# Optimization experiments

Hardware: AMD Instinct MI355X
Metric: run time of the kernel (lower is better)

The kernel has to match this reference:

```python
import jax, jax.numpy as jnp
import numpy as np

NHEAD = 8
LN_EPS = 1e-5


def _layernorm(x, g, b):
    mu = jnp.mean(x, -1, keepdims=True)
    var = jnp.mean((x - mu) ** 2, -1, keepdims=True)
    return (x - mu) / jnp.sqrt(var + LN_EPS) * g + b


def _sparse_attn(q, k, v, P):
    # Topology: P queries attend to P keys; G queries attend to P keys + self.
    # q,k,v: [B,H,L,dh], keys/values restricted to pcpt block [B,H,P,dh]
    dh = q.shape[-1]
    scale = 1.0 / jnp.sqrt(jnp.asarray(dh, q.dtype))
    kp, vp = k[:, :, :P], v[:, :, :P]
    S = jnp.einsum('bhld,bhpd->bhlp', q, kp) * scale  # [B,H,L,P]
    # pcpt queries: plain softmax over P keys
    out_p = jnp.einsum('bhqp,bhpd->bhqd', jax.nn.softmax(S[:, :, :P], axis=-1), vp)
    # gen queries: P keys + own diagonal key
    qg, kg, vg = q[:, :, P:], k[:, :, P:], v[:, :, P:]
    Sg = S[:, :, P:]                                   # [B,H,G,P]
    dlog = jnp.sum(qg * kg, -1) * scale                # [B,H,G] diagonal logits
    m = jnp.maximum(jnp.max(Sg, -1), dlog)
    eg = jnp.exp(Sg - m[..., None])
    ed = jnp.exp(dlog - m)
    den = jnp.sum(eg, -1) + ed
    out_g = (jnp.einsum('bhgp,bhpd->bhgd', eg, vp) + ed[..., None] * vg) / den[..., None]
    return jnp.concatenate([out_p, out_g], axis=2)     # [B,H,L,dh]


def _forward(pcpt, gen, Wqkv, bqkv, Wo, bo, W1, b1, W2, b2, g1, beta1, g2, beta2):
    P = pcpt.shape[1]
    x = jnp.concatenate([pcpt, gen], axis=1)           # [B,L,d]
    B, L, d = x.shape
    dh = d // NHEAD
    for i in range(Wqkv.shape[0]):  # post-norm layers
        qkv = (x @ Wqkv[i] + bqkv[i]).reshape(B, L, 3, NHEAD, dh)
        q = jnp.transpose(qkv[:, :, 0], (0, 2, 1, 3))
        k = jnp.transpose(qkv[:, :, 1], (0, 2, 1, 3))
        v = jnp.transpose(qkv[:, :, 2], (0, 2, 1, 3))
        a = _sparse_attn(q, k, v, P)
        a = jnp.transpose(a, (0, 2, 1, 3)).reshape(B, L, d)
        a = a @ Wo[i] + bo[i]
        x = _layernorm(x + a, g1[i], beta1[i])
        h = jax.nn.relu(x @ W1[i] + b1[i]) @ W2[i] + b2[i]
        x = _layernorm(x + h, g2[i], beta2[i])
    return x


def setup_inputs() -> dict:
    key = jax.random.key(0)
    ks = jax.random.split(key, 16)
    B, P, G, d, ff, Lyr = 4, 1024, 1024, 512, 2048, 4
    s = 0.02
    f32 = jnp.float32
    return {
        'pcpt_total_embs': jax.random.normal(ks[0], (B, P, d), f32),
        'gen_total_embs': jax.random.normal(ks[1], (B, G, d), f32),
        'src_key_padding_mask': jnp.zeros((B, P + G), bool),
        'Wqkv': jax.random.normal(ks[2], (Lyr, d, 3 * d), f32) * s,
        'bqkv': jnp.zeros((Lyr, 3 * d), f32),
        'Wo': jax.random.normal(ks[3], (Lyr, d, d), f32) * s,
        'bo': jnp.zeros((Lyr, d), f32),
        'W1': jax.random.normal(ks[4], (Lyr, d, ff), f32) * s,
        'b1': jnp.zeros((Lyr, ff), f32),
        'W2': jax.random.normal(ks[5], (Lyr, ff, d), f32) * s,
        'b2': jnp.zeros((Lyr, d), f32),
        'g1': jnp.ones((Lyr, d), f32),
        'beta1': jnp.zeros((Lyr, d), f32),
        'g2': jnp.ones((Lyr, d), f32),
        'beta2': jnp.zeros((Lyr, d), f32),
    }


def reference(pcpt_total_embs, gen_total_embs, src_key_padding_mask, Wqkv, bqkv, Wo, bo, W1, b1, W2, b2, g1, beta1, g2, beta2):
    P = pcpt_total_embs.shape[1]
    x = _forward(pcpt_total_embs, gen_total_embs, Wqkv, bqkv, Wo, bo, W1, b1, W2, b2, g1, beta1, g2, beta2)
    return x[:, :P], x[:, P:]
```

## Files before the change

### kernel.cpp

```cpp
#include <hip/hip_runtime.h>
#include <hip/hip_bf16.h>

#define B_ 4
#define P_ 1024
#define G_ 1024
#define L_ 2048
#define D_ 512
#define FF_ 2048
#define H_ 8
#define DH_ 64
#define LAYERS_ 4
#define LN_EPS_ 1e-5f

typedef __attribute__((ext_vector_type(8))) short bf16x8;
typedef __attribute__((ext_vector_type(4))) float f32x4;

__device__ __forceinline__ ushort f2b(float f) {
  unsigned u = __float_as_uint(f);
  unsigned r = (u + 0x7fffu + ((u >> 16) & 1u)) >> 16;
  return (ushort)r;
}
__device__ __forceinline__ float b2f(ushort u) {
  return __uint_as_float(((unsigned)u) << 16);
}

__device__ __forceinline__ void gld16(const ushort* g, ushort* l) {
  __builtin_amdgcn_global_load_lds(
      (const __attribute__((address_space(1))) void*)g,
      (__attribute__((address_space(3))) void*)l, 16, 0, 0);
}

__global__ __launch_bounds__(256) void concat_kernel(const float* __restrict__ p,
    const float* __restrict__ g, float* __restrict__ x, ushort* __restrict__ xb)
{
  const int LD4 = L_*D_/4, PD4 = P_*D_/4;
  int i = blockIdx.x*256 + threadIdx.x;
  int b = i / LD4, r = i - b*LD4;
  float4 v;
  if (r < PD4) v = ((const float4*)p)[(size_t)b*PD4 + r];
  else         v = ((const float4*)g)[(size_t)b*PD4 + (r-PD4)];
  ((float4*)x)[i] = v;
  ushort4 h; h.x=f2b(v.x); h.y=f2b(v.y); h.z=f2b(v.z); h.w=f2b(v.w);
  ((ushort4*)xb)[i] = h;
}

__global__ __launch_bounds__(256) void writeout_kernel(const float* __restrict__ x,
    float* __restrict__ out)
{
  const int LD4 = L_*D_/4, PD4 = P_*D_/4, HALF = B_*PD4;
  int i = blockIdx.x*256 + threadIdx.x;
  int half = (i >= HALF) ? 1 : 0;
  int r = i - half*HALF;
  int b = r / PD4, q = r - b*PD4;
  ((float4*)out)[i] = ((const float4*)x)[(size_t)b*LD4 + half*PD4 + q];
}

__global__ __launch_bounds__(256) void wconv_kernel(const float* __restrict__ src,
    ushort* __restrict__ dst, int K, int N)
{
  __shared__ float tile[32][33];
  int n0 = blockIdx.x*32, k0 = blockIdx.y*32, l = blockIdx.z;
  src += (size_t)l*K*N; dst += (size_t)l*K*N;
  int tx = threadIdx.x & 31, ty = threadIdx.x >> 5;
  #pragma unroll
  for (int u=0;u<4;++u) tile[ty+8*u][tx] = src[(size_t)(k0+ty+8*u)*N + n0+tx];
  __syncthreads();
  #pragma unroll
  for (int u=0;u<4;++u) dst[(size_t)(n0+ty+8*u)*K + k0+tx] = f2b(tile[tx][ty+8*u]);
}

template<int BN_, int RELU, int RES, int OUTBF>
__global__ __launch_bounds__(256) void mgemm(
    const ushort* __restrict__ A, const ushort* __restrict__ Bt,
    const float* __restrict__ bias, const float* __restrict__ res,
    void* __restrict__ Cout, int M, int N, int K)
{
  constexpr int MI = (BN_ == 128) ? 4 : 2;
  constexpr int BL = BN_ / 32;
  __shared__ ushort As[128*64];
  __shared__ ushort Bs[BN_*64];
  int t = threadIdx.x;
  int lane = t & 63, w = t >> 6;
  int wm = (BN_ == 128) ? (w >> 1) * 64 : w * 32;
  int wn = (BN_ == 128) ? (w & 1) * 64 : 0;
  int m0 = blockIdx.x * 128, n0 = blockIdx.y * BN_;

  f32x4 acc[MI][4] = {};

  int rbase = t >> 3;
  int cch   = (t & 7) ^ ((t >> 3) & 7);
  const ushort* Ag = A  + (size_t)(m0 + rbase)*K + cch*8;
  const ushort* Bg = Bt + (size_t)(n0 + rbase)*K + cch*8;
  ushort* Asl = As + t*8;
  ushort* Bsl = Bs + t*8;
  const size_t rowK32 = (size_t)32 * K;

  int fr = lane & 15, fq = lane >> 4;
  int swr[2];
  swr[0] = ((0*4 + fq) ^ (fr & 7)) * 8;
  swr[1] = ((1*4 + fq) ^ (fr & 7)) * 8;
  const ushort* Ard = As + (wm + fr)*64;
  const ushort* Brd = Bs + (wn + fr)*64;

  for (int k0 = 0; k0 < K; k0 += 64) {
    __syncthreads();
    #pragma unroll
    for (int L = 0; L < 4; ++L)  gld16(Ag + L*rowK32, Asl + L*2048);
    #pragma unroll
    for (int L = 0; L < BL; ++L) gld16(Bg + L*rowK32, Bsl + L*2048);
    Ag += 64; Bg += 64;
    __syncthreads();
    #pragma unroll
    for (int s = 0; s < 2; ++s) {
      int sw = swr[s];
      bf16x8 af[MI], bfr[4];
      #pragma unroll
      for (int i=0;i<MI;++i) af[i]  = *(const bf16x8*)(Ard + i*16*64 + sw);
      #pragma unroll
      for (int j=0;j<4;++j)  bfr[j] = *(const bf16x8*)(Brd + j*16*64 + sw);
      #pragma unroll
      for (int i=0;i<MI;++i)
        #pragma unroll
        for (int j=0;j<4;++j)
          acc[i][j] = __builtin_amdgcn_mfma_f32_16x16x32_bf16(af[i], bfr[j], acc[i][j], 0, 0, 0);
    }
  }

  int ncol = lane & 15;
  int rquad = (lane >> 4) * 4;
  #pragma unroll
  for (int j=0;j<4;++j) {
    int n = n0 + wn + j*16 + ncol;
    float bv = bias[n];
    #pragma unroll
    for (int i=0;i<MI;++i) {
      int mbase = m0 + wm + i*16 + rquad;
      #pragma unroll
      for (int r=0;r<4;++r) {
        int m = mbase + r;
        float c = acc[i][j][r] + bv;
        if (RES) c += res[(size_t)m*N + n];
        if (RELU) c = fmaxf(c, 0.f);
        if (OUTBF) ((ushort*)Cout)[(size_t)m*N + n] = f2b(c);
        else       ((float*)Cout)[(size_t)m*N + n] = c;
      }
    }
  }
}

__global__ __launch_bounds__(256) void mgemm_qkv(
    const ushort* __restrict__ A,
    const ushort* __restrict__ Bt,
    const float* __restrict__ bias,
    ushort* __restrict__ qb,
    ushort* __restrict__ kb,
    ushort* __restrict__ vtb)
{
  const int K = D_;
  __shared__ ushort As[128*64];
  __shared__ ushort Bs[128*64];
  int t = threadIdx.x;
  int lane = t & 63, w = t >> 6;
  int wm = (w >> 1) * 64, wn = (w & 1) * 64;
  int m0 = blockIdx.x * 128, n0 = blockIdx.y * 128;

  f32x4 acc[4][4] = {};

  int rbase = t >> 3;
  int cch   = (t & 7) ^ ((t >> 3) & 7);
  const ushort* Ag = A  + (size_t)(m0 + rbase)*K + cch*8;
  const ushort* Bg = Bt + (size_t)(n0 + rbase)*K + cch*8;
  ushort* Asl = As + t*8;
  ushort* Bsl = Bs + t*8;
  const size_t rowK32 = (size_t)32 * K;

  int fr = lane & 15, fq = lane >> 4;
  int swr[2];
  swr[0] = ((0*4 + fq) ^ (fr & 7)) * 8;
  swr[1] = ((1*4 + fq) ^ (fr & 7)) * 8;
  const ushort* Ard = As + (wm + fr)*64;
  const ushort* Brd = Bs + (wn + fr)*64;

  for (int k0 = 0; k0 < K; k0 += 64) {
    __syncthreads();
    #pragma unroll
    for (int L = 0; L < 4; ++L) gld16(Ag + L*rowK32, Asl + L*2048);
    #pragma unroll
    for (int L = 0; L < 4; ++L) gld16(Bg + L*rowK32, Bsl + L*2048);
    Ag += 64; Bg += 64;
    __syncthreads();
    #pragma unroll
    for (int s = 0; s < 2; ++s) {
      int sw = swr[s];
      bf16x8 af[4], bfr[4];
      #pragma unroll
      for (int i=0;i<4;++i) af[i]  = *(const bf16x8*)(Ard + i*16*64 + sw);
      #pragma unroll
      for (int j=0;j<4;++j) bfr[j] = *(const bf16x8*)(Brd + j*16*64 + sw);
      #pragma unroll
      for (int i=0;i<4;++i)
        #pragma unroll
        for (int j=0;j<4;++j)
          acc[i][j] = __builtin_amdgcn_mfma_f32_16x16x32_bf16(af[i], bfr[j], acc[i][j], 0, 0, 0);
    }
  }

  int ncol = lane & 15;
  int rquad = (lane >> 4) * 4;
  #pragma unroll
  for (int j=0;j<4;++j) {
    int n = n0 + wn + j*16 + ncol;
    float bv = bias[n];
    int part = n >> 9;
    int wi = n & 511;
    int h = wi >> 6, d = wi & 63;
    #pragma unroll
    for (int i=0;i<4;++i) {
      int mbase = m0 + wm + i*16 + rquad;
      #pragma unroll
      for (int r=0;r<4;++r) {
        int m = mbase + r;
        int b = m >> 11, l = m & 2047;
        int bh = b*H_ + h;
        float cv = acc[i][j][r] + bv;
        if (part == 0) cv *= 0.125f;
        ushort c = f2b(cv);
        if (part == 0)      qb[((size_t)bh*L_ + l)*DH_ + d] = c;
        else if (part == 1) kb[((size_t)bh*L_ + l)*DH_ + d] = c;
        else                vtb[((size_t)bh*DH_ + d)*L_ + l] = c;
      }
    }
  }
}

__global__ __launch_bounds__(256) void attn_mfma(
    const ushort* __restrict__ qb, const ushort* __restrict__ kb,
    const ushort* __restrict__ vtb, ushort* __restrict__ outa)
{
  __shared__ ushort Qs[64*72];
  __shared__ ushort Ks[64*72];
  __shared__ ushort Vts[64*72];
  __shared__ ushort Ps[4*16*72];
  __shared__ float dls[64];

  int t = threadIdx.x;
  int lane = t & 63, w = t >> 6;
  int qt = blockIdx.x & 31;
  int h  = (blockIdx.x >> 5) & 7;
  int b  = blockIdx.x >> 8;
  int l0 = qt * 64;
  bool isgen = (l0 >= P_);
  int bh = b*H_ + h;

  const ushort* qg  = qb  + ((size_t)bh*L_ + l0)*DH_;
  const ushort* kgb = kb  + (size_t)bh*L_*DH_;
  const ushort* vtg = vtb + (size_t)bh*DH_*L_;

  int sr = t >> 3, sc = (t & 7) * 8;

  {
    uint4 x0 = *(const uint4*)(qg + (size_t)sr*DH_ + sc);
    uint4 x1 = *(const uint4*)(qg + (size_t)(sr+32)*DH_ + sc);
    *(uint4*)(Qs + sr*72 + sc) = x0;
    *(uint4*)(Qs + (sr+32)*72 + sc) = x1;
  }
  __syncthreads();

  int fr = lane & 15, fq = lane >> 4;
  bf16x8 qf[2];
  qf[0] = *(const bf16x8*)(Qs + (16*w + fr)*72 + 0*32 + fq*8);
  qf[1] = *(const bf16x8*)(Qs + (16*w + fr)*72 + 1*32 + fq*8);

  float den[4] = {0.f, 0.f, 0.f, 0.f};
  f32x4 o[4] = {};

  ushort* Pw = Ps + w*16*72;

  uint4 pk0 = *(const uint4*)(kgb + (size_t)sr*DH_ + sc);
  uint4 pk1 = *(const uint4*)(kgb + (size_t)(sr+32)*DH_ + sc);
  uint4 pv0 = *(const uint4*)(vtg + (size_t)sr*L_ + sc);
  uint4 pv1 = *(const uint4*)(vtg + (size_t)(sr+32)*L_ + sc);

  for (int kt = 0; kt < 16; ++kt) {
    __syncthreads();
    *(uint4*)(Ks + sr*72 + sc) = pk0;
    *(uint4*)(Ks + (sr+32)*72 + sc) = pk1;
    *(uint4*)(Vts + sr*72 + sc) = pv0;
    *(uint4*)(Vts + (sr+32)*72 + sc) = pv1;
    __syncthreads();

    if (kt < 15) {
      int p1 = (kt + 1) * 64;
      pk0 = *(const uint4*)(kgb + (size_t)(p1+sr)*DH_ + sc);
      pk1 = *(const uint4*)(kgb + (size_t)(p1+sr+32)*DH_ + sc);
      pv0 = *(const uint4*)(vtg + (size_t)sr*L_ + p1 + sc);
      pv1 = *(const uint4*)(vtg + (size_t)(sr+32)*L_ + p1 + sc);
    }

    f32x4 sc4[4] = {};
    #pragma unroll
    for (int s=0;s<2;++s) {
      #pragma unroll
      for (int j=0;j<4;++j) {
        bf16x8 kf = *(const bf16x8*)(Ks + (j*16 + fr)*72 + s*32 + fq*8);
        sc4[j] = __builtin_amdgcn_mfma_f32_16x16x32_bf16(qf[s], kf, sc4[j], 0, 0, 0);
      }
    }

    #pragma unroll
    for (int r=0;r<4;++r) {
      float e0 = __expf(sc4[0][r]);
      float e1 = __expf(sc4[1][r]);
      float e2 = __expf(sc4[2][r]);
      float e3 = __expf(sc4[3][r]);
      den[r] += (e0+e1) + (e2+e3);
      Pw[(fq*4+r)*72 +  0 + fr] = (ushort)(__float_as_uint(e0) >> 16);
      Pw[(fq*4+r)*72 + 16 + fr] = (ushort)(__float_as_uint(e1) >> 16);
      Pw[(fq*4+r)*72 + 32 + fr] = (ushort)(__float_as_uint(e2) >> 16);
      Pw[(fq*4+r)*72 + 48 + fr] = (ushort)(__float_as_uint(e3) >> 16);
    }
    asm volatile("s_waitcnt lgkmcnt(0)" ::: "memory");

    #pragma unroll
    for (int s=0;s<2;++s) {
      bf16x8 pf = *(const bf16x8*)(Pw + fr*72 + s*32 + fq*8);
      #pragma unroll
      for (int j=0;j<4;++j) {
        bf16x8 vf = *(const bf16x8*)(Vts + (j*16 + fr)*72 + s*32 + fq*8);
        o[j] = __builtin_amdgcn_mfma_f32_16x16x32_bf16(pf, vf, o[j], 0, 0, 0);
      }
    }
  }

  #pragma unroll
  for (int r=0;r<4;++r) {
    float d = den[r];
    d += __shfl_xor(d, 1, 16);
    d += __shfl_xor(d, 2, 16);
    d += __shfl_xor(d, 4, 16);
    d += __shfl_xor(d, 8, 16);
    den[r] = d;
  }

  if (isgen) {
    __syncthreads();
    {
      uint4 k0v = *(const uint4*)(kgb + (size_t)(l0+sr)*DH_ + sc);
      uint4 k1v = *(const uint4*)(kgb + (size_t)(l0+sr+32)*DH_ + sc);
      uint4 v0v = *(const uint4*)(vtg + (size_t)sr*L_ + l0 + sc);
      uint4 v1v = *(const uint4*)(vtg + (size_t)(sr+32)*L_ + l0 + sc);
      *(uint4*)(Ks + sr*72 + sc) = k0v;
      *(uint4*)(Ks + (sr+32)*72 + sc) = k1v;
      *(uint4*)(Vts + sr*72 + sc) = v0v;
      *(uint4*)(Vts + (sr+32)*72 + sc) = v1v;
    }
    __syncthreads();
    {
      int row = t >> 2, part = t & 3;
      float dsum = 0.f;
      #pragma unroll
      for (int u=0;u<16;++u) {
        int d = part*16 + u;
        dsum = fmaf(b2f(Qs[row*72+d]), b2f(Ks[row*72+d]), dsum);
      }
      dsum += __shfl_xor(dsum, 1, 4);
      dsum += __shfl_xor(dsum, 2, 4);
      if (part == 0) dls[row] = dsum;
    }
    __syncthreads();
    #pragma unroll
    for (int r=0;r<4;++r) {
      int rr = 16*w + fq*4 + r;
      float ed = __expf(dls[rr]);
      den[r] += ed;
      #pragma unroll
      for (int j=0;j<4;++j) {
        float vv = b2f(Vts[(j*16 + fr)*72 + rr]);
        o[j][r] += ed*vv;
      }
    }
  }

  #pragma unroll
  for (int r=0;r<4;++r) {
    float inv = 1.f / den[r];
    int l = l0 + 16*w + fq*4 + r;
    #pragma unroll
    for (int j=0;j<4;++j)
      outa[((size_t)b*L_ + l)*D_ + h*DH_ + j*16 + fr] = f2b(o[j][r]*inv);
  }
}

__global__ __launch_bounds__(64) void ln_kernel(const float* __restrict__ y,
    const float* __restrict__ gw, const float* __restrict__ bw,
    float* __restrict__ x, ushort* __restrict__ xb)
{
  int row = blockIdx.x, t = threadIdx.x;
  const float4* yr = (const float4*)(y + (size_t)row*D_);
  float4 v0 = yr[t], v1 = yr[t+64];
  float s = v0.x+v0.y+v0.z+v0.w + v1.x+v1.y+v1.z+v1.w;
  for (int off=32; off>0; off>>=1) s += __shfl_down(s, off, 64);
  s = __shfl(s, 0, 64);
  float mu = s * (1.f/D_);
  float dx;
  float q = 0.f;
  dx=v0.x-mu; q+=dx*dx; dx=v0.y-mu; q+=dx*dx; dx=v0.z-mu; q+=dx*dx; dx=v0.w-mu; q+=dx*dx;
  dx=v1.x-mu; q+=dx*dx; dx=v1.y-mu; q+=dx*dx; dx=v1.z-mu; q+=dx*dx; dx=v1.w-mu; q+=dx*dx;
  for (int off=32; off>0; off>>=1) q += __shfl_down(q, off, 64);
  q = __shfl(q, 0, 64);
  float rinv = rsqrtf(q*(1.f/D_) + LN_EPS_);
  const float4* g4 = (const float4*)gw;
  const float4* b4 = (const float4*)bw;
  float4 gv0=g4[t], gv1=g4[t+64], bv0=b4[t], bv1=b4[t+64];
  float4 o0, o1;
  o0.x=(v0.x-mu)*rinv*gv0.x+bv0.x; o0.y=(v0.y-mu)*rinv*gv0.y+bv0.y;
  o0.z=(v0.z-mu)*rinv*gv0.z+bv0.z; o0.w=(v0.w-mu)*rinv*gv0.w+bv0.w;
  o1.x=(v1.x-mu)*rinv*gv1.x+bv1.x; o1.y=(v1.y-mu)*rinv*gv1.y+bv1.y;
  o1.z=(v1.z-mu)*rinv*gv1.z+bv1.z; o1.w=(v1.w-mu)*rinv*gv1.w+bv1.w;
  float4* xr = (float4*)(x + (size_t)row*D_);
  xr[t]=o0; xr[t+64]=o1;
  ushort4 h0, h1;
  h0.x=f2b(o0.x); h0.y=f2b(o0.y); h0.z=f2b(o0.z); h0.w=f2b(o0.w);
  h1.x=f2b(o1.x); h1.y=f2b(o1.y); h1.z=f2b(o1.z); h1.w=f2b(o1.w);
  ushort4* xbr = (ushort4*)(xb + (size_t)row*D_);
  xbr[t]=h0; xbr[t+64]=h1;
}

extern "C" void kernel_launch(void* const* d_in, const int* in_sizes, int n_in,
                              void* d_out, int out_size, void* d_ws, size_t ws_size,
                              hipStream_t stream) {
  const float* pcpt = (const float*)d_in[0];
  const float* gen  = (const float*)d_in[1];
  const float* Wqkv = (const float*)d_in[3];
  const float* bqkv = (const float*)d_in[4];
  const float* Wo   = (const float*)d_in[5];
  const float* bo   = (const float*)d_in[6];
  const float* W1   = (const float*)d_in[7];
  const float* b1   = (const float*)d_in[8];
  const float* W2   = (const float*)d_in[9];
  const float* b2   = (const float*)d_in[10];
  const float* g1   = (const float*)d_in[11];
  const float* be1  = (const float*)d_in[12];
  const float* g2   = (const float*)d_in[13];
  const float* be2  = (const float*)d_in[14];
  float* out = (float*)d_out;

  const size_t XD  = (size_t)B_*L_*D_;
  const size_t HKV = (size_t)B_*H_*L_*DH_;
  const size_t HFF = (size_t)B_*L_*FF_;

  float*  xbuf = (float*)d_ws;
  ushort* xbf  = (ushort*)(xbuf + XD);
  ushort* region = xbf + XD;
  ushort* qb  = region;
  ushort* kb  = region + HKV;
  ushort* vtb = region + 2*HKV;
  ushort* hbf = region;
  ushort* abf = region + HFF;
  ushort* wb  = abf + XD;
  ushort* wqkv_b = wb;
  ushort* wo_b   = wqkv_b + (size_t)4*3*D_*D_;
  ushort* w1_b   = wo_b   + (size_t)4*D_*D_;
  ushort* w2_b   = w1_b   + (size_t)4*FF_*D_;
  float*  ybuf = out;

  const int M = B_*L_;

  wconv_kernel<<<dim3(3*D_/32, D_/32, 4), 256, 0, stream>>>(Wqkv, wqkv_b, D_, 3*D_);
  wconv_kernel<<<dim3(D_/32,   D_/32, 4), 256, 0, stream>>>(Wo,   wo_b,   D_, D_);
  wconv_kernel<<<dim3(FF_/32,  D_/32, 4), 256, 0, stream>>>(W1,   w1_b,   D_, FF_);
  wconv_kernel<<<dim3(D_/32,  FF_/32, 4), 256, 0, stream>>>(W2,   w2_b,   FF_, D_);

  concat_kernel<<<4096, 256, 0, stream>>>(pcpt, gen, xbuf, xbf);

  for (int i = 0; i < LAYERS_; ++i) {
    const ushort* wqkv_i = wqkv_b + (size_t)i*3*D_*D_;
    const ushort* wo_i   = wo_b   + (size_t)i*D_*D_;
    const ushort* w1_i   = w1_b   + (size_t)i*FF_*D_;
    const ushort* w2_i   = w2_b   + (size_t)i*D_*FF_;
    const float* bqkv_i = bqkv + (size_t)i*3*D_;
    const float* bo_i   = bo   + (size_t)i*D_;
    const float* b1_i   = b1   + (size_t)i*FF_;
    const float* b2_i   = b2   + (size_t)i*D_;
    const float* g1_i   = g1   + (size_t)i*D_;
    const float* be1_i  = be1  + (size_t)i*D_;
    const float* g2_i   = g2   + (size_t)i*D_;
    const float* be2_i  = be2  + (size_t)i*D_;

    mgemm_qkv<<<dim3(M/128, 3*D_/128), 256, 0, stream>>>(
        xbf, wqkv_i, bqkv_i, qb, kb, vtb);

    attn_mfma<<<B_*H_*(L_/64), 256, 0, stream>>>(qb, kb, vtb, abf);

    mgemm<64,0,1,0><<<dim3(M/128, D_/64), 256, 0, stream>>>(
        abf, wo_i, bo_i, xbuf, ybuf, M, D_, D_);

    ln_kernel<<<M, 64, 0, stream>>>(ybuf, g1_i, be1_i, xbuf, xbf);

    mgemm<128,1,0,1><<<dim3(M/128, FF_/128), 256, 0, stream>>>(
        xbf, w1_i, b1_i, nullptr, hbf, M, FF_, D_);

    mgemm<64,0,1,0><<<dim3(M/128, D_/64), 256, 0, stream>>>(
        hbf, w2_i, b2_i, xbuf, ybuf, M, D_, FF_);

    ln_kernel<<<M, 64, 0, stream>>>(ybuf, g2_i, be2_i, xbuf, xbf);
  }

  writeout_kernel<<<4096, 256, 0, stream>>>(xbuf, out);
}
```

Before: 790.0 us.

## Load attention K/V fragments straight from global memory, dropping LDS staging

The attention kernel no longer stages Q, K and V^T tiles through shared memory. Each wave now loads its MFMA operand fragments directly from global memory, which removes the per-tile __syncthreads barriers and cuts LDS use. The diagonal logit for generated queries is now computed with an MFMA plus a lane shuffle instead of a scalar LDS dot product, and a min-blocks hint of 4 is added to launch bounds. The cost is that all four waves in a block re-fetch the same K/V data and rely on the caches, and global-load latency is no longer hidden by the explicit register prefetch.

```diff
diff --git a/kernel.cpp b/kernel.cpp
--- a/kernel.cpp
+++ b/kernel.cpp
@@ -233,15 +233,11 @@
   }
 }
 
-__global__ __launch_bounds__(256) void attn_mfma(
+__global__ __launch_bounds__(256, 4) void attn_mfma(
     const ushort* __restrict__ qb, const ushort* __restrict__ kb,
     const ushort* __restrict__ vtb, ushort* __restrict__ outa)
 {
-  __shared__ ushort Qs[64*72];
-  __shared__ ushort Ks[64*72];
-  __shared__ ushort Vts[64*72];
   __shared__ ushort Ps[4*16*72];
-  __shared__ float dls[64];
 
   int t = threadIdx.x;
   int lane = t & 63, w = t >> 6;
@@ -256,56 +252,39 @@
   const ushort* kgb = kb  + (size_t)bh*L_*DH_;
   const ushort* vtg = vtb + (size_t)bh*DH_*L_;
 
-  int sr = t >> 3, sc = (t & 7) * 8;
-
-  {
-    uint4 x0 = *(const uint4*)(qg + (size_t)sr*DH_ + sc);
-    uint4 x1 = *(const uint4*)(qg + (size_t)(sr+32)*DH_ + sc);
-    *(uint4*)(Qs + sr*72 + sc) = x0;
-    *(uint4*)(Qs + (sr+32)*72 + sc) = x1;
-  }
-  __syncthreads();
-
   int fr = lane & 15, fq = lane >> 4;
+
   bf16x8 qf[2];
-  qf[0] = *(const bf16x8*)(Qs + (16*w + fr)*72 + 0*32 + fq*8);
-  qf[1] = *(const bf16x8*)(Qs + (16*w + fr)*72 + 1*32 + fq*8);
+  qf[0] = *(const bf16x8*)(qg + (size_t)(16*w + fr)*DH_ + 0*32 + fq*8);
+  qf[1] = *(const bf16x8*)(qg + (size_t)(16*w + fr)*DH_ + 1*32 + fq*8);
 
   float den[4] = {0.f, 0.f, 0.f, 0.f};
   f32x4 o[4] = {};
 
   ushort* Pw = Ps + w*16*72;
 
-  uint4 pk0 = *(const uint4*)(kgb + (size_t)sr*DH_ + sc);
-  uint4 pk1 = *(const uint4*)(kgb + (size_t)(sr+32)*DH_ + sc);
-  uint4 pv0 = *(const uint4*)(vtg + (size_t)sr*L_ + sc);
-  uint4 pv1 = *(const uint4*)(vtg + (size_t)(sr+32)*L_ + sc);
-
   for (int kt = 0; kt < 16; ++kt) {
-    __syncthreads();
-    *(uint4*)(Ks + sr*72 + sc) = pk0;
-    *(uint4*)(Ks + (sr+32)*72 + sc) = pk1;
-    *(uint4*)(Vts + sr*72 + sc) = pv0;
-    *(uint4*)(Vts + (sr+32)*72 + sc) = pv1;
-    __syncthreads();
-
-    if (kt < 15) {
-      int p1 = (kt + 1) * 64;
-      pk0 = *(const uint4*)(kgb + (size_t)(p1+sr)*DH_ + sc);
-      pk1 = *(const uint4*)(kgb + (size_t)(p1+sr+32)*DH_ + sc);
-      pv0 = *(const uint4*)(vtg + (size_t)sr*L_ + p1 + sc);
-      pv1 = *(const uint4*)(vtg + (size_t)(sr+32)*L_ + p1 + sc);
-    }
+    const ushort* kp = kgb + (size_t)kt*64*DH_;
+    const ushort* vp = vtg + kt*64;
+
+    bf16x8 kf0[4], kf1[4], vf0[4], vf1[4];
+    #pragma unroll
+    for (int j=0;j<4;++j) kf0[j] = *(const bf16x8*)(kp + (size_t)(j*16+fr)*DH_ + 0*32 + fq*8);
+    #pragma unroll
+    for (int j=0;j<4;++j) kf1[j] = *(const bf16x8*)(kp + (size_t)(j*16+fr)*DH_ + 1*32 + fq*8);
+    #pragma unroll
+    for (int j=0;j<4;++j) vf0[j] = *(const bf16x8*)(vp + (size_t)(j*16+fr)*L_ + 0*32 + fq*8);
 
     f32x4 sc4[4] = {};
     #pragma unroll
-    for (int s=0;s<2;++s) {
-      #pragma unroll
-      for (int j=0;j<4;++j) {
-        bf16x8 kf = *(const bf16x8*)(Ks + (j*16 + fr)*72 + s*32 + fq*8);
-        sc4[j] = __builtin_amdgcn_mfma_f32_16x16x32_bf16(qf[s], kf, sc4[j], 0, 0, 0);
-      }
-    }
+    for (int j=0;j<4;++j)
+      sc4[j] = __builtin_amdgcn_mfma_f32_16x16x32_bf16(qf[0], kf0[j], sc4[j], 0, 0, 0);
+    #pragma unroll
+    for (int j=0;j<4;++j)
+      sc4[j] = __builtin_amdgcn_mfma_f32_16x16x32_bf16(qf[1], kf1[j], sc4[j], 0, 0, 0);
+
+    #pragma unroll
+    for (int j=0;j<4;++j) vf1[j] = *(const bf16x8*)(vp + (size_t)(j*16+fr)*L_ + 1*32 + fq*8);
 
     #pragma unroll
     for (int r=0;r<4;++r) {
@@ -321,14 +300,15 @@
     }
     asm volatile("s_waitcnt lgkmcnt(0)" ::: "memory");
 
-    #pragma unroll
-    for (int s=0;s<2;++s) {
-      bf16x8 pf = *(const bf16x8*)(Pw + fr*72 + s*32 + fq*8);
-      #pragma unroll
-      for (int j=0;j<4;++j) {
-        bf16x8 vf = *(const bf16x8*)(Vts + (j*16 + fr)*72 + s*32 + fq*8);
-        o[j] = __builtin_amdgcn_mfma_f32_16x16x32_bf16(pf, vf, o[j], 0, 0, 0);
-      }
+    {
+      bf16x8 pf0 = *(const bf16x8*)(Pw + fr*72 + 0*32 + fq*8);
+      #pragma unroll
+      for (int j=0;j<4;++j)
+        o[j] = __builtin_amdgcn_mfma_f32_16x16x32_bf16(pf0, vf0[j], o[j], 0, 0, 0);
+      bf16x8 pf1 = *(const bf16x8*)(Pw + fr*72 + 1*32 + fq*8);
+      #pragma unroll
+      for (int j=0;j<4;++j)
+        o[j] = __builtin_amdgcn_mfma_f32_16x16x32_bf16(pf1, vf1[j], o[j], 0, 0, 0);
     }
   }
 
@@ -343,39 +323,23 @@
   }
 
   if (isgen) {
-    __syncthreads();
+    f32x4 dsc = {};
     {
-      uint4 k0v = *(const uint4*)(kgb + (size_t)(l0+sr)*DH_ + sc);
-      uint4 k1v = *(const uint4*)(kgb + (size_t)(l0+sr+32)*DH_ + sc);
-      uint4 v0v = *(const uint4*)(vtg + (size_t)sr*L_ + l0 + sc);
-      uint4 v1v = *(const uint4*)(vtg + (size_t)(sr+32)*L_ + l0 + sc);
-      *(uint4*)(Ks + sr*72 + sc) = k0v;
-      *(uint4*)(Ks + (sr+32)*72 + sc) = k1v;
-      *(uint4*)(Vts + sr*72 + sc) = v0v;
-      *(uint4*)(Vts + (sr+32)*72 + sc) = v1v;
-    }
-    __syncthreads();
-    {
-      int row = t >> 2, part = t & 3;
-      float dsum = 0.f;
-      #pragma unroll
-      for (int u=0;u<16;++u) {
-        int d = part*16 + u;
-        dsum = fmaf(b2f(Qs[row*72+d]), b2f(Ks[row*72+d]), dsum);
-      }
-      dsum += __shfl_xor(dsum, 1, 4);
-      dsum += __shfl_xor(dsum, 2, 4);
-      if (part == 0) dls[row] = dsum;
-    }
-    __syncthreads();
+      bf16x8 kd0 = *(const bf16x8*)(kgb + (size_t)(l0 + 16*w + fr)*DH_ + 0*32 + fq*8);
+      dsc = __builtin_amdgcn_mfma_f32_16x16x32_bf16(qf[0], kd0, dsc, 0, 0, 0);
+      bf16x8 kd1 = *(const bf16x8*)(kgb + (size_t)(l0 + 16*w + fr)*DH_ + 1*32 + fq*8);
+      dsc = __builtin_amdgcn_mfma_f32_16x16x32_bf16(qf[1], kd1, dsc, 0, 0, 0);
+    }
     #pragma unroll
     for (int r=0;r<4;++r) {
-      int rr = 16*w + fq*4 + r;
-      float ed = __expf(dls[rr]);
+      int m = fq*4 + r;
+      float dl = __shfl(dsc[r], fq*16 + m);
+      float ed = __expf(dl);
       den[r] += ed;
+      int l = l0 + 16*w + m;
       #pragma unroll
       for (int j=0;j<4;++j) {
-        float vv = b2f(Vts[(j*16 + fr)*72 + rr]);
+        float vv = b2f(vtg[(size_t)(j*16 + fr)*L_ + l]);
         o[j][r] += ed*vv;
       }
     }
```

After: 1.106 ms. 1.4x slower.
